# Kernel optimization log

Measured on AMD Instinct MI355X. Metric: run time of the kernel, lower is better.

## Reference

```python
import jax, jax.numpy as jnp
import numpy as np

B, S, I, C, P = 64, 14, 32, 10, 4   # batch, spatial, in-caps/pos, classes, pose size
ROUTINGS = 3
EPS = 1e-9


def setup_inputs() -> dict:
    key = jax.random.key(0)
    k1, k2, k3, k4, k5 = jax.random.split(key, 5)
    return {
        "inputs_pose": jax.random.normal(k1, (B, S, S, I, P, P), jnp.float32),
        "inputs_activation": jax.random.uniform(k2, (B, S, S, I), jnp.float32),
        "w": jax.random.normal(k3, (1, I, C, P, P), jnp.float32),
        "beta_v": jax.random.normal(k4, (1, C), jnp.float32) * 0.1,
        "beta_a": jax.random.normal(k5, (1, C), jnp.float32) * 0.1,
    }


def _em_routing(votes, i_act, beta_v, beta_a, routings):
    # votes: [B, N, C, 16], i_act: [B, N]
    Bn, N, Cc, D = votes.shape
    rr = jnp.full((Bn, N, Cc, 1), 1.0 / Cc, votes.dtype)  # uniform init assignments
    bv = beta_v.reshape(1, 1, Cc, 1)
    ba = beta_a.reshape(1, 1, Cc, 1)
    it_min, it_max = 1.0, min(float(routings), 3.0)  # inverse-temperature schedule
    o_mean = o_act = None
    for it in range(routings):
        inv_temp = it_min + (it_max - it_min) * it / max(1.0, routings - 1.0)
        # --- M step ---
        rr_p = rr * i_act[:, :, None, None]                        # [B,N,C,1]
        rr_sum = jnp.sum(rr_p, axis=1, keepdims=True)              # [B,1,C,1]
        o_mean = jnp.sum(rr_p * votes, axis=1, keepdims=True) / rr_sum   # [B,1,C,16]
        o_var = jnp.sum(rr_p * jnp.square(votes - o_mean), axis=1, keepdims=True) / rr_sum
        o_stdv = jnp.sqrt(o_var)                                   # [B,1,C,16]
        cost = jnp.sum((bv + jnp.log(o_stdv + EPS)) * rr_sum, axis=-1, keepdims=True)  # [B,1,C,1]
        o_act = jax.nn.sigmoid(inv_temp * (ba - cost))             # [B,1,C,1]
        # --- E step (skipped on last iteration) ---
        if it < routings - 1:
            logp = (-jnp.sum(jnp.square(votes - o_mean) / (2.0 * jnp.square(o_stdv) + EPS),
                             axis=-1, keepdims=True)
                    - jnp.sum(jnp.log(o_stdv + EPS), axis=-1, keepdims=True))  # [B,N,C,1]
            zz = jnp.log(o_act + EPS) + logp
            rr = jax.nn.softmax(zz, axis=2)
    return o_mean[:, 0], o_act[:, 0, :, 0]  # [B,C,16], [B,C]


def reference(inputs_pose, inputs_activation, w, beta_v, beta_a):
    # mat_transform: votes[b,h,w,i,c] = pose[b,h,w,i] @ W[i,c]   (4x4 matmuls)
    votes = jnp.einsum('bhwipq,icqr->bhwicpr', inputs_pose, w[0])
    votes = votes.reshape(B, S, S, I, C, P * P)
    # coordinate addition: scaled (row+0.5)/S onto pose element 0, col onto element 1
    coord = (jnp.arange(S, dtype=votes.dtype) + 0.5) / S
    votes = votes.at[..., 0].add(coord[None, :, None, None, None])
    votes = votes.at[..., 1].add(coord[None, None, :, None, None])
    votes = votes.reshape(B, S * S * I, C, P * P)
    acts = inputs_activation.reshape(B, S * S * I)
    o_mean, o_act = _em_routing(votes, acts, beta_v, beta_a, ROUTINGS)
    pose = o_mean.reshape(B, C, P, P)
    return pose, o_act
```

## Files before the change

kernel.cpp:

```cpp
#include <hip/hip_runtime.h>
#include <math.h>

#define Bsz 64
#define Ssz 14
#define Isz 32
#define Csz 10
#define Dsz 16
#define Nsz (Ssz*Ssz*Isz)
#define EPSF 1e-9f

#define CH   448
#define NCH  14
#define BLK  640
#define ITER (CH/64)

__device__ __forceinline__ void vote_reg(const float* p, const float* Wr,
                                         float chh, float cww, float* v)
{
#pragma unroll
    for (int pr = 0; pr < 4; ++pr)
#pragma unroll
        for (int r = 0; r < 4; ++r)
            v[pr*4+r] = p[pr*4+0]*Wr[0*4+r] + p[pr*4+1]*Wr[1*4+r]
                      + p[pr*4+2]*Wr[2*4+r] + p[pr*4+3]*Wr[3*4+r];
    v[0] += chh;
    v[1] += cww;
}

__device__ __forceinline__ void load_W_regs(const float* __restrict__ w,
                                            int lane, int c, float* Wr)
{
    const float4* ws = reinterpret_cast<const float4*>(w + (((lane & 31)*Csz + c) * Dsz));
    float4 b0 = ws[0], b1 = ws[1], b2 = ws[2], b3 = ws[3];
    Wr[0]=b0.x; Wr[1]=b0.y; Wr[2]=b0.z; Wr[3]=b0.w;
    Wr[4]=b1.x; Wr[5]=b1.y; Wr[6]=b1.z; Wr[7]=b1.w;
    Wr[8]=b2.x; Wr[9]=b2.y; Wr[10]=b2.z; Wr[11]=b2.w;
    Wr[12]=b3.x; Wr[13]=b3.y; Wr[14]=b3.z; Wr[15]=b3.w;
}

__device__ __forceinline__ void load_pose_lds(const float* Pl, int nl, float* p)
{
    const float4* pp = reinterpret_cast<const float4*>(Pl + nl*Dsz);
    float4 a0 = pp[0], a1 = pp[1], a2 = pp[2], a3 = pp[3];
    p[0]=a0.x; p[1]=a0.y; p[2]=a0.z; p[3]=a0.w;
    p[4]=a1.x; p[5]=a1.y; p[6]=a1.z; p[7]=a1.w;
    p[8]=a2.x; p[9]=a2.y; p[10]=a2.z; p[11]=a2.w;
    p[12]=a3.x; p[13]=a3.y; p[14]=a3.z; p[15]=a3.w;
}

__global__ __launch_bounds__(BLK) void m0_kernel(
    const float* __restrict__ pose,
    const float* __restrict__ act,
    const float* __restrict__ w,
    float* __restrict__ partials)
{
    const int b = blockIdx.x, chunk = blockIdx.y;
    const int tid = threadIdx.x, c = tid >> 6, lane = tid & 63;
    const int base = chunk * CH;

    __shared__ float Pl[CH*Dsz];

    const float* poseb = pose + (size_t)b * Nsz * Dsz;
    {
        const float4* gp = reinterpret_cast<const float4*>(poseb + (size_t)base * Dsz);
        float4* lp = reinterpret_cast<float4*>(Pl);
        for (int t = tid; t < CH*4; t += BLK) lp[t] = gp[t];
    }

    float Wr[16];
    load_W_regs(w, lane, c, Wr);
    __syncthreads();

    float s0 = 0.f, s1[Dsz], s2[Dsz];
#pragma unroll
    for (int d = 0; d < Dsz; ++d) { s1[d] = 0.f; s2[d] = 0.f; }

    const float* actb = act + (size_t)b * Nsz;

    for (int it = 0; it < ITER; ++it) {
        const int nl = it*64 + lane;
        const int n  = base + nl;
        float p[16];
        load_pose_lds(Pl, nl, p);
        int hw = n >> 5;
        int wc = hw % Ssz, hr = hw / Ssz;
        float wgt = actb[n] * (1.0f/Csz);
        float v[16];
        vote_reg(p, Wr, (hr+0.5f)*(1.0f/Ssz), (wc+0.5f)*(1.0f/Ssz), v);
        s0 += wgt;
#pragma unroll
        for (int d = 0; d < Dsz; ++d) {
            float wv = wgt * v[d];
            s1[d] += wv;
            s2[d] += wv * v[d];
        }
    }

#pragma unroll
    for (int m = 32; m >= 1; m >>= 1) {
        s0 += __shfl_xor(s0, m);
#pragma unroll
        for (int d = 0; d < Dsz; ++d) {
            s1[d] += __shfl_xor(s1[d], m);
            s2[d] += __shfl_xor(s2[d], m);
        }
    }
    if (lane == 0) {
        float* pt = partials + ((size_t)(b*Csz + c)*NCH + chunk)*33;
        pt[0] = s0;
#pragma unroll
        for (int d = 0; d < Dsz; ++d) { pt[1+d] = s1[d]; pt[17+d] = s2[d]; }
    }
}

__global__ __launch_bounds__(BLK) void em_kernel(
    const float* __restrict__ pose,
    const float* __restrict__ act,
    const float* __restrict__ w,
    const float* __restrict__ beta_v,
    const float* __restrict__ beta_a,
    const float* __restrict__ part_in,
    float* __restrict__ part_out,
    float inv_temp_prev)
{
    const int b = blockIdx.x, chunk = blockIdx.y;
    const int tid = threadIdx.x, wv = tid >> 6, lane = tid & 63;
    const int base = chunk * CH;

    __shared__ float Pl[CH*Dsz];
    __shared__ float zz[CH][11];
    __shared__ float Sv[Csz][33];
    __shared__ float prm[Csz][33];
    __shared__ float lg[Csz][16];

    const float* poseb = pose + (size_t)b * Nsz * Dsz;
    {
        const float4* gp = reinterpret_cast<const float4*>(poseb + (size_t)base * Dsz);
        float4* lp = reinterpret_cast<float4*>(Pl);
        for (int t = tid; t < CH*4; t += BLK) lp[t] = gp[t];
    }

    float Wr[16];
    load_W_regs(w, lane, wv, Wr);

    if (tid < Csz*33) {
        int c = tid / 33, j = tid - c*33;
        const float* pp = part_in + ((size_t)(b*Csz + c)*NCH)*33 + j;
        float s = 0.f;
        for (int ch2 = 0; ch2 < NCH; ++ch2) s += pp[ch2*33];
        Sv[c][j] = s;
    }
    __syncthreads();
    if (tid < Csz*Dsz) {
        int c = tid >> 4, d = tid & 15;
        float S0 = Sv[c][0];
        float mn  = Sv[c][1+d] / S0;
        float var = fmaxf(Sv[c][17+d] / S0 - mn*mn, 0.f);
        prm[c][d]    = mn;
        prm[c][16+d] = 1.f / (2.f*var + EPSF);
        lg[c][d]     = __logf(sqrtf(var) + EPSF);
    }
    __syncthreads();
    if (tid < Csz) {
        int c = tid;
        float sumlog = 0.f;
#pragma unroll
        for (int d = 0; d < Dsz; ++d) sumlog += lg[c][d];
        float cost = Sv[c][0] * (16.f * beta_v[c] + sumlog);
        float oact = 1.f / (1.f + __expf(-inv_temp_prev * (beta_a[c] - cost)));
        prm[c][32] = __logf(oact + EPSF) - sumlog;
    }
    __syncthreads();

    {
        float mn[Dsz], iv[Dsz];
#pragma unroll
        for (int d = 0; d < Dsz; ++d) { mn[d] = prm[wv][d]; iv[d] = prm[wv][16+d]; }
        float Kc = prm[wv][32];

        for (int it = 0; it < ITER; ++it) {
            const int nl = it*64 + lane;
            const int n  = base + nl;
            float p[16];
            load_pose_lds(Pl, nl, p);
            int hw = n >> 5;
            int wc = hw % Ssz, hr = hw / Ssz;
            float v[16];
            vote_reg(p, Wr, (hr+0.5f)*(1.0f/Ssz), (wc+0.5f)*(1.0f/Ssz), v);
            float quad = 0.f;
#pragma unroll
            for (int d = 0; d < Dsz; ++d) {
                float dv = v[d] - mn[d];
                quad += dv * dv * iv[d];
            }
            zz[nl][wv] = Kc - quad;
        }
    }
    __syncthreads();

    if (tid < CH) {
        const int n = base + tid;
        float z[Csz];
#pragma unroll
        for (int c = 0; c < Csz; ++c) z[c] = zz[tid][c];
        float zmax = z[0];
#pragma unroll
        for (int c = 1; c < Csz; ++c) zmax = fmaxf(zmax, z[c]);
        float zsum = 0.f;
#pragma unroll
        for (int c = 0; c < Csz; ++c) { z[c] = __expf(z[c] - zmax); zsum += z[c]; }
        float sc = __fdividef(act[(size_t)b*Nsz + n], zsum);
#pragma unroll
        for (int c = 0; c < Csz; ++c) zz[tid][c] = z[c] * sc;
    }
    __syncthreads();

    float s0 = 0.f, s1[Dsz], s2[Dsz];
#pragma unroll
    for (int d = 0; d < Dsz; ++d) { s1[d] = 0.f; s2[d] = 0.f; }

    for (int it = 0; it < ITER; ++it) {
        const int nl = it*64 + lane;
        const int n  = base + nl;
        float p[16];
        load_pose_lds(Pl, nl, p);
        int hw = n >> 5;
        int wc = hw % Ssz, hr = hw / Ssz;
        float wgt = zz[nl][wv];
        float v[16];
        vote_reg(p, Wr, (hr+0.5f)*(1.0f/Ssz), (wc+0.5f)*(1.0f/Ssz), v);
        s0 += wgt;
#pragma unroll
        for (int d = 0; d < Dsz; ++d) {
            float wvv = wgt * v[d];
            s1[d] += wvv;
            s2[d] += wvv * v[d];
        }
    }

#pragma unroll
    for (int m = 32; m >= 1; m >>= 1) {
        s0 += __shfl_xor(s0, m);
#pragma unroll
        for (int d = 0; d < Dsz; ++d) {
            s1[d] += __shfl_xor(s1[d], m);
            s2[d] += __shfl_xor(s2[d], m);
        }
    }
    if (lane == 0) {
        float* pt = part_out + ((size_t)(b*Csz + wv)*NCH + chunk)*33;
        pt[0] = s0;
#pragma unroll
        for (int d = 0; d < Dsz; ++d) { pt[1+d] = s1[d]; pt[17+d] = s2[d]; }
    }
}

__global__ __launch_bounds__(64) void fin_kernel(
    const float* __restrict__ partials,
    const float* __restrict__ beta_v,
    const float* __restrict__ beta_a,
    float* __restrict__ out,
    float inv_temp)
{
    const int bc = blockIdx.x * 64 + threadIdx.x;
    if (bc >= Bsz*Csz) return;
    const int c = bc % Csz;

    float S[33];
#pragma unroll
    for (int j = 0; j < 33; ++j) S[j] = 0.f;
    const float* pb = partials + (size_t)bc * NCH * 33;
    for (int ch2 = 0; ch2 < NCH; ++ch2)
#pragma unroll
        for (int j = 0; j < 33; ++j) S[j] += pb[ch2*33 + j];

    float S0 = S[0], rS0 = 1.f / S0;
    float sumlog = 0.f;
    float* om = out + (size_t)bc * Dsz;
#pragma unroll
    for (int d = 0; d < Dsz; ++d) {
        float mn  = S[1+d] * rS0;
        float var = fmaxf(S[17+d] * rS0 - mn*mn, 0.f);
        sumlog += __logf(sqrtf(var) + EPSF);
        om[d] = mn;
    }
    float cost = S0 * (16.f * beta_v[c] + sumlog);
    float oact = 1.f / (1.f + __expf(-inv_temp * (beta_a[c] - cost)));
    out[Bsz*Csz*Dsz + bc] = oact;
}

extern "C" void kernel_launch(void* const* d_in, const int* in_sizes, int n_in,
                              void* d_out, int out_size, void* d_ws, size_t ws_size,
                              hipStream_t stream)
{
    const float* pose = (const float*)d_in[0];
    const float* act  = (const float*)d_in[1];
    const float* w    = (const float*)d_in[2];
    const float* bv   = (const float*)d_in[3];
    const float* ba   = (const float*)d_in[4];
    float* out = (float*)d_out;

    float* partA = (float*)d_ws;
    float* partB = partA + (size_t)Bsz*Csz*NCH*33;

    dim3 grid(Bsz, NCH);

    m0_kernel<<<grid, BLK, 0, stream>>>(pose, act, w, partA);
    em_kernel<<<grid, BLK, 0, stream>>>(pose, act, w, bv, ba, partA, partB, 1.0f);
    em_kernel<<<grid, BLK, 0, stream>>>(pose, act, w, bv, ba, partB, partA, 2.0f);
    fin_kernel<<<(Bsz*Csz + 63)/64, 64, 0, stream>>>(partA, bv, ba, out, 3.0f);
}
```

Baseline: 238.8 us.

## Fold final reduction into last EM kernel via tickets, transpose LDS pose layout

Removes the separate finalisation kernel. The last EM launch now uses a per-batch atomic ticket counter so that the last-arriving block reduces the partials and writes the pose means and activations. The shared-memory pose tile is stored as four planes indexed by float4 slot, so each lane reads consecutive float4s and bank conflicts drop. The quadratic form is also split into four independent accumulators to shorten the dependency chain. The cost is atomics, thread fences, and a ticket array in the workspace that m0 resets.

```diff
diff --git a/kernel.cpp b/kernel.cpp
--- a/kernel.cpp
+++ b/kernel.cpp
@@ -38,10 +38,19 @@
     Wr[12]=b3.x; Wr[13]=b3.y; Wr[14]=b3.z; Wr[15]=b3.w;
 }
 
+__device__ __forceinline__ void stage_pose(const float* __restrict__ poseb,
+                                           int base, int tid, float* Pl)
+{
+    const float4* gp = reinterpret_cast<const float4*>(poseb + (size_t)base * Dsz);
+    float4* lp = reinterpret_cast<float4*>(Pl);
+    for (int f = tid; f < CH*4; f += BLK)
+        lp[(f & 3)*CH + (f >> 2)] = gp[f];
+}
+
 __device__ __forceinline__ void load_pose_lds(const float* Pl, int nl, float* p)
 {
-    const float4* pp = reinterpret_cast<const float4*>(Pl + nl*Dsz);
-    float4 a0 = pp[0], a1 = pp[1], a2 = pp[2], a3 = pp[3];
+    const float4* q = reinterpret_cast<const float4*>(Pl);
+    float4 a0 = q[0*CH + nl], a1 = q[1*CH + nl], a2 = q[2*CH + nl], a3 = q[3*CH + nl];
     p[0]=a0.x; p[1]=a0.y; p[2]=a0.z; p[3]=a0.w;
     p[4]=a1.x; p[5]=a1.y; p[6]=a1.z; p[7]=a1.w;
     p[8]=a2.x; p[9]=a2.y; p[10]=a2.z; p[11]=a2.w;
@@ -52,20 +61,19 @@
     const float* __restrict__ pose,
     const float* __restrict__ act,
     const float* __restrict__ w,
-    float* __restrict__ partials)
+    float* __restrict__ partials,
+    int* __restrict__ tickets)
 {
     const int b = blockIdx.x, chunk = blockIdx.y;
     const int tid = threadIdx.x, c = tid >> 6, lane = tid & 63;
     const int base = chunk * CH;
 
-    __shared__ float Pl[CH*Dsz];
+    if (b == 0 && chunk == 0 && tid < Bsz) tickets[tid] = 0;
+
+    __shared__ float Pl[4*CH*4];
 
     const float* poseb = pose + (size_t)b * Nsz * Dsz;
-    {
-        const float4* gp = reinterpret_cast<const float4*>(poseb + (size_t)base * Dsz);
-        float4* lp = reinterpret_cast<float4*>(Pl);
-        for (int t = tid; t < CH*4; t += BLK) lp[t] = gp[t];
-    }
+    stage_pose(poseb, base, tid, Pl);
 
     float Wr[16];
     load_W_regs(w, lane, c, Wr);
@@ -121,24 +129,24 @@
     const float* __restrict__ beta_a,
     const float* __restrict__ part_in,
     float* __restrict__ part_out,
-    float inv_temp_prev)
+    float inv_temp_prev,
+    int final_it, float inv_temp_final,
+    int* __restrict__ tickets,
+    float* __restrict__ out)
 {
     const int b = blockIdx.x, chunk = blockIdx.y;
     const int tid = threadIdx.x, wv = tid >> 6, lane = tid & 63;
     const int base = chunk * CH;
 
-    __shared__ float Pl[CH*Dsz];
+    __shared__ float Pl[4*CH*4];
     __shared__ float zz[CH][11];
     __shared__ float Sv[Csz][33];
     __shared__ float prm[Csz][33];
     __shared__ float lg[Csz][16];
+    __shared__ int isLast;
 
     const float* poseb = pose + (size_t)b * Nsz * Dsz;
-    {
-        const float4* gp = reinterpret_cast<const float4*>(poseb + (size_t)base * Dsz);
-        float4* lp = reinterpret_cast<float4*>(Pl);
-        for (int t = tid; t < CH*4; t += BLK) lp[t] = gp[t];
-    }
+    stage_pose(poseb, base, tid, Pl);
 
     float Wr[16];
     load_W_regs(w, lane, wv, Wr);
@@ -187,13 +195,15 @@
             int wc = hw % Ssz, hr = hw / Ssz;
             float v[16];
             vote_reg(p, Wr, (hr+0.5f)*(1.0f/Ssz), (wc+0.5f)*(1.0f/Ssz), v);
-            float quad = 0.f;
-#pragma unroll
-            for (int d = 0; d < Dsz; ++d) {
-                float dv = v[d] - mn[d];
-                quad += dv * dv * iv[d];
+            float qa = 0.f, qb = 0.f, qc = 0.f, qd = 0.f;
+#pragma unroll
+            for (int d = 0; d < 4; ++d) {
+                float d0 = v[d]    - mn[d];    qa += d0*d0*iv[d];
+                float d1 = v[4+d]  - mn[4+d];  qb += d1*d1*iv[4+d];
+                float d2 = v[8+d]  - mn[8+d];  qc += d2*d2*iv[8+d];
+                float d3 = v[12+d] - mn[12+d]; qd += d3*d3*iv[12+d];
             }
-            zz[nl][wv] = Kc - quad;
+            zz[nl][wv] = Kc - ((qa+qb)+(qc+qd));
         }
     }
     __syncthreads();
@@ -253,40 +263,44 @@
 #pragma unroll
         for (int d = 0; d < Dsz; ++d) { pt[1+d] = s1[d]; pt[17+d] = s2[d]; }
     }
-}
-
-__global__ __launch_bounds__(64) void fin_kernel(
-    const float* __restrict__ partials,
-    const float* __restrict__ beta_v,
-    const float* __restrict__ beta_a,
-    float* __restrict__ out,
-    float inv_temp)
-{
-    const int bc = blockIdx.x * 64 + threadIdx.x;
-    if (bc >= Bsz*Csz) return;
-    const int c = bc % Csz;
-
-    float S[33];
-#pragma unroll
-    for (int j = 0; j < 33; ++j) S[j] = 0.f;
-    const float* pb = partials + (size_t)bc * NCH * 33;
-    for (int ch2 = 0; ch2 < NCH; ++ch2)
-#pragma unroll
-        for (int j = 0; j < 33; ++j) S[j] += pb[ch2*33 + j];
-
-    float S0 = S[0], rS0 = 1.f / S0;
-    float sumlog = 0.f;
-    float* om = out + (size_t)bc * Dsz;
-#pragma unroll
-    for (int d = 0; d < Dsz; ++d) {
-        float mn  = S[1+d] * rS0;
-        float var = fmaxf(S[17+d] * rS0 - mn*mn, 0.f);
-        sumlog += __logf(sqrtf(var) + EPSF);
-        om[d] = mn;
-    }
-    float cost = S0 * (16.f * beta_v[c] + sumlog);
-    float oact = 1.f / (1.f + __expf(-inv_temp * (beta_a[c] - cost)));
-    out[Bsz*Csz*Dsz + bc] = oact;
+
+    if (final_it) {
+        __threadfence();
+        if (tid == 0) {
+            int r = atomicAdd(&tickets[b], 1);
+            isLast = (r == NCH - 1);
+        }
+        __syncthreads();
+        if (isLast) {
+            __threadfence();
+            if (tid < Csz*33) {
+                int c = tid / 33, j = tid - c*33;
+                const float* pp = part_out + ((size_t)(b*Csz + c)*NCH)*33 + j;
+                float s = 0.f;
+                for (int ch2 = 0; ch2 < NCH; ++ch2) s += pp[ch2*33];
+                Sv[c][j] = s;
+            }
+            __syncthreads();
+            if (tid < Csz*Dsz) {
+                int c = tid >> 4, d = tid & 15;
+                float S0 = Sv[c][0];
+                float mn  = Sv[c][1+d] / S0;
+                float var = fmaxf(Sv[c][17+d] / S0 - mn*mn, 0.f);
+                lg[c][d] = __logf(sqrtf(var) + EPSF);
+                out[(size_t)(b*Csz + c)*Dsz + d] = mn;
+            }
+            __syncthreads();
+            if (tid < Csz) {
+                int c = tid;
+                float sumlog = 0.f;
+#pragma unroll
+                for (int d = 0; d < Dsz; ++d) sumlog += lg[c][d];
+                float cost = Sv[c][0] * (16.f * beta_v[c] + sumlog);
+                float oact = 1.f / (1.f + __expf(-inv_temp_final * (beta_a[c] - cost)));
+                out[Bsz*Csz*Dsz + b*Csz + c] = oact;
+            }
+        }
+    }
 }
 
 extern "C" void kernel_launch(void* const* d_in, const int* in_sizes, int n_in,
@@ -302,11 +316,13 @@
 
     float* partA = (float*)d_ws;
     float* partB = partA + (size_t)Bsz*Csz*NCH*33;
+    int* tickets = (int*)(partB + (size_t)Bsz*Csz*NCH*33);
 
     dim3 grid(Bsz, NCH);
 
-    m0_kernel<<<grid, BLK, 0, stream>>>(pose, act, w, partA);
-    em_kernel<<<grid, BLK, 0, stream>>>(pose, act, w, bv, ba, partA, partB, 1.0f);
-    em_kernel<<<grid, BLK, 0, stream>>>(pose, act, w, bv, ba, partB, partA, 2.0f);
-    fin_kernel<<<(Bsz*Csz + 63)/64, 64, 0, stream>>>(partA, bv, ba, out, 3.0f);
-}
+    m0_kernel<<<grid, BLK, 0, stream>>>(pose, act, w, partA, tickets);
+    em_kernel<<<grid, BLK, 0, stream>>>(pose, act, w, bv, ba, partA, partB,
+                                        1.0f, 0, 0.0f, tickets, out);
+    em_kernel<<<grid, BLK, 0, stream>>>(pose, act, w, bv, ba, partB, partA,
+                                        2.0f, 1, 3.0f, tickets, out);
+}
```

Result: slower. 403.2 us (+68.8%).

## Use SoA pose layout in LDS, shorten wave reductions, parallelize final reduce

Applied to the files above, without the earlier changes.

Pose staging in shared memory now uses a component-major float4 layout, so consecutive lanes read consecutive float4s and LDS bank conflicts drop. The full 64-lane shuffle reduction becomes a 3-step reduction, and 8 partial copies per wave go to global memory, which moves the remaining summation into the consumers. The quadratic-form accumulation is split across four independent accumulators to add ILP. fin_kernel now uses one block per (b,c) with threads summing columns in parallel. The trade-off is 8x more partial data to write and read in each next stage.

```diff
diff --git a/kernel.cpp b/kernel.cpp
--- a/kernel.cpp
+++ b/kernel.cpp
@@ -13,6 +13,7 @@
 #define NCH  14
 #define BLK  640
 #define ITER (CH/64)
+#define NCOPY 8
 
 __device__ __forceinline__ void vote_reg(const float* p, const float* Wr,
                                          float chh, float cww, float* v)
@@ -38,14 +39,43 @@
     Wr[12]=b3.x; Wr[13]=b3.y; Wr[14]=b3.z; Wr[15]=b3.w;
 }
 
+__device__ __forceinline__ void stage_pose(const float* __restrict__ poseb,
+                                           int base, int tid, float* Pl)
+{
+    const float4* gp = reinterpret_cast<const float4*>(poseb + (size_t)base * Dsz);
+    float4* lp = reinterpret_cast<float4*>(Pl);
+    for (int f = tid; f < CH*4; f += BLK)
+        lp[(f & 3)*CH + (f >> 2)] = gp[f];
+}
+
 __device__ __forceinline__ void load_pose_lds(const float* Pl, int nl, float* p)
 {
-    const float4* pp = reinterpret_cast<const float4*>(Pl + nl*Dsz);
-    float4 a0 = pp[0], a1 = pp[1], a2 = pp[2], a3 = pp[3];
+    const float4* q = reinterpret_cast<const float4*>(Pl);
+    float4 a0 = q[0*CH + nl], a1 = q[1*CH + nl], a2 = q[2*CH + nl], a3 = q[3*CH + nl];
     p[0]=a0.x; p[1]=a0.y; p[2]=a0.z; p[3]=a0.w;
     p[4]=a1.x; p[5]=a1.y; p[6]=a1.z; p[7]=a1.w;
     p[8]=a2.x; p[9]=a2.y; p[10]=a2.z; p[11]=a2.w;
     p[12]=a3.x; p[13]=a3.y; p[14]=a3.z; p[15]=a3.w;
+}
+
+__device__ __forceinline__ void reduce_store(float s0, float* s1, float* s2,
+                                             float* __restrict__ pt, int lane)
+{
+#pragma unroll
+    for (int m = 1; m <= 4; m <<= 1) {
+        s0 += __shfl_xor(s0, m);
+#pragma unroll
+        for (int d = 0; d < Dsz; ++d) {
+            s1[d] += __shfl_xor(s1[d], m);
+            s2[d] += __shfl_xor(s2[d], m);
+        }
+    }
+    if ((lane & 7) == 0) {
+        float* po = pt + (lane >> 3) * 33;
+        po[0] = s0;
+#pragma unroll
+        for (int d = 0; d < Dsz; ++d) { po[1+d] = s1[d]; po[17+d] = s2[d]; }
+    }
 }
 
 __global__ __launch_bounds__(BLK) void m0_kernel(
@@ -58,14 +88,10 @@
     const int tid = threadIdx.x, c = tid >> 6, lane = tid & 63;
     const int base = chunk * CH;
 
-    __shared__ float Pl[CH*Dsz];
+    __shared__ float Pl[4*CH*4];
 
     const float* poseb = pose + (size_t)b * Nsz * Dsz;
-    {
-        const float4* gp = reinterpret_cast<const float4*>(poseb + (size_t)base * Dsz);
-        float4* lp = reinterpret_cast<float4*>(Pl);
-        for (int t = tid; t < CH*4; t += BLK) lp[t] = gp[t];
-    }
+    stage_pose(poseb, base, tid, Pl);
 
     float Wr[16];
     load_W_regs(w, lane, c, Wr);
@@ -96,21 +122,8 @@
         }
     }
 
-#pragma unroll
-    for (int m = 32; m >= 1; m >>= 1) {
-        s0 += __shfl_xor(s0, m);
-#pragma unroll
-        for (int d = 0; d < Dsz; ++d) {
-            s1[d] += __shfl_xor(s1[d], m);
-            s2[d] += __shfl_xor(s2[d], m);
-        }
-    }
-    if (lane == 0) {
-        float* pt = partials + ((size_t)(b*Csz + c)*NCH + chunk)*33;
-        pt[0] = s0;
-#pragma unroll
-        for (int d = 0; d < Dsz; ++d) { pt[1+d] = s1[d]; pt[17+d] = s2[d]; }
-    }
+    float* pt = partials + ((size_t)((b*Csz + c)*NCH + chunk))*NCOPY*33;
+    reduce_store(s0, s1, s2, pt, lane);
 }
 
 __global__ __launch_bounds__(BLK) void em_kernel(
@@ -127,27 +140,23 @@
     const int tid = threadIdx.x, wv = tid >> 6, lane = tid & 63;
     const int base = chunk * CH;
 
-    __shared__ float Pl[CH*Dsz];
+    __shared__ float Pl[4*CH*4];
     __shared__ float zz[CH][11];
     __shared__ float Sv[Csz][33];
     __shared__ float prm[Csz][33];
     __shared__ float lg[Csz][16];
 
     const float* poseb = pose + (size_t)b * Nsz * Dsz;
-    {
-        const float4* gp = reinterpret_cast<const float4*>(poseb + (size_t)base * Dsz);
-        float4* lp = reinterpret_cast<float4*>(Pl);
-        for (int t = tid; t < CH*4; t += BLK) lp[t] = gp[t];
-    }
+    stage_pose(poseb, base, tid, Pl);
 
     float Wr[16];
     load_W_regs(w, lane, wv, Wr);
 
     if (tid < Csz*33) {
         int c = tid / 33, j = tid - c*33;
-        const float* pp = part_in + ((size_t)(b*Csz + c)*NCH)*33 + j;
+        const float* pp = part_in + ((size_t)(b*Csz + c)*NCH)*NCOPY*33 + j;
         float s = 0.f;
-        for (int ch2 = 0; ch2 < NCH; ++ch2) s += pp[ch2*33];
+        for (int t = 0; t < NCH*NCOPY; ++t) s += pp[t*33];
         Sv[c][j] = s;
     }
     __syncthreads();
@@ -187,13 +196,15 @@
             int wc = hw % Ssz, hr = hw / Ssz;
             float v[16];
             vote_reg(p, Wr, (hr+0.5f)*(1.0f/Ssz), (wc+0.5f)*(1.0f/Ssz), v);
-            float quad = 0.f;
-#pragma unroll
-            for (int d = 0; d < Dsz; ++d) {
-                float dv = v[d] - mn[d];
-                quad += dv * dv * iv[d];
+            float qa = 0.f, qb = 0.f, qc = 0.f, qd = 0.f;
+#pragma unroll
+            for (int d = 0; d < 4; ++d) {
+                float d0 = v[d]    - mn[d];    qa += d0*d0*iv[d];
+                float d1 = v[4+d]  - mn[4+d];  qb += d1*d1*iv[4+d];
+                float d2 = v[8+d]  - mn[8+d];  qc += d2*d2*iv[8+d];
+                float d3 = v[12+d] - mn[12+d]; qd += d3*d3*iv[12+d];
             }
-            zz[nl][wv] = Kc - quad;
+            zz[nl][wv] = Kc - ((qa+qb)+(qc+qd));
         }
     }
     __syncthreads();
@@ -238,21 +249,8 @@
         }
     }
 
-#pragma unroll
-    for (int m = 32; m >= 1; m >>= 1) {
-        s0 += __shfl_xor(s0, m);
-#pragma unroll
-        for (int d = 0; d < Dsz; ++d) {
-            s1[d] += __shfl_xor(s1[d], m);
-            s2[d] += __shfl_xor(s2[d], m);
-        }
-    }
-    if (lane == 0) {
-        float* pt = part_out + ((size_t)(b*Csz + wv)*NCH + chunk)*33;
-        pt[0] = s0;
-#pragma unroll
-        for (int d = 0; d < Dsz; ++d) { pt[1+d] = s1[d]; pt[17+d] = s2[d]; }
-    }
+    float* pt = part_out + ((size_t)((b*Csz + wv)*NCH + chunk))*NCOPY*33;
+    reduce_store(s0, s1, s2, pt, lane);
 }
 
 __global__ __launch_bounds__(64) void fin_kernel(
@@ -262,31 +260,36 @@
     float* __restrict__ out,
     float inv_temp)
 {
-    const int bc = blockIdx.x * 64 + threadIdx.x;
-    if (bc >= Bsz*Csz) return;
+    const int bc = blockIdx.x;
     const int c = bc % Csz;
-
-    float S[33];
-#pragma unroll
-    for (int j = 0; j < 33; ++j) S[j] = 0.f;
-    const float* pb = partials + (size_t)bc * NCH * 33;
-    for (int ch2 = 0; ch2 < NCH; ++ch2)
-#pragma unroll
-        for (int j = 0; j < 33; ++j) S[j] += pb[ch2*33 + j];
-
-    float S0 = S[0], rS0 = 1.f / S0;
-    float sumlog = 0.f;
-    float* om = out + (size_t)bc * Dsz;
-#pragma unroll
-    for (int d = 0; d < Dsz; ++d) {
-        float mn  = S[1+d] * rS0;
-        float var = fmaxf(S[17+d] * rS0 - mn*mn, 0.f);
-        sumlog += __logf(sqrtf(var) + EPSF);
-        om[d] = mn;
-    }
-    float cost = S0 * (16.f * beta_v[c] + sumlog);
-    float oact = 1.f / (1.f + __expf(-inv_temp * (beta_a[c] - cost)));
-    out[Bsz*Csz*Dsz + bc] = oact;
+    const int tid = threadIdx.x;
+
+    __shared__ float S[33];
+    __shared__ float lgs[16];
+
+    if (tid < 33) {
+        const float* pp = partials + (size_t)bc * NCH * NCOPY * 33 + tid;
+        float s = 0.f;
+        for (int t = 0; t < NCH*NCOPY; ++t) s += pp[t*33];
+        S[tid] = s;
+    }
+    __syncthreads();
+    if (tid < Dsz) {
+        float S0 = S[0];
+        float mn  = S[1+tid] / S0;
+        float var = fmaxf(S[17+tid] / S0 - mn*mn, 0.f);
+        lgs[tid] = __logf(sqrtf(var) + EPSF);
+        out[(size_t)bc * Dsz + tid] = mn;
+    }
+    __syncthreads();
+    if (tid == 0) {
+        float sumlog = 0.f;
+#pragma unroll
+        for (int d = 0; d < Dsz; ++d) sumlog += lgs[d];
+        float cost = S[0] * (16.f * beta_v[c] + sumlog);
+        float oact = 1.f / (1.f + __expf(-inv_temp * (beta_a[c] - cost)));
+        out[Bsz*Csz*Dsz + bc] = oact;
+    }
 }
 
 extern "C" void kernel_launch(void* const* d_in, const int* in_sizes, int n_in,
@@ -301,12 +304,12 @@
     float* out = (float*)d_out;
 
     float* partA = (float*)d_ws;
-    float* partB = partA + (size_t)Bsz*Csz*NCH*33;
+    float* partB = partA + (size_t)Bsz*Csz*NCH*NCOPY*33;
 
     dim3 grid(Bsz, NCH);
 
     m0_kernel<<<grid, BLK, 0, stream>>>(pose, act, w, partA);
     em_kernel<<<grid, BLK, 0, stream>>>(pose, act, w, bv, ba, partA, partB, 1.0f);
     em_kernel<<<grid, BLK, 0, stream>>>(pose, act, w, bv, ba, partB, partA, 2.0f);
-    fin_kernel<<<(Bsz*Csz + 63)/64, 64, 0, stream>>>(partA, bv, ba, out, 3.0f);
-}
+    fin_kernel<<<Bsz*Csz, 64, 0, stream>>>(partA, bv, ba, out, 3.0f);
+}
```

Result: no change. 237.6 us (-0.5%).
